# Kernel tuning notes

Hardware: AMD Instinct MI355X
Metric: run time of the kernel (lower is better)

## Reference

```python
import jax, jax.numpy as jnp
import numpy as np

ALPHA = 8.3  # depth similarity sharpness, F_D = exp(-alpha*|D(p0)-D(pn)|) (depth-aware CNN)
PAD, STRIDE, DIL, KH, KW = 1, 1, 1, 3, 3


def setup_inputs() -> dict:
    key = jax.random.key(0)
    k1, k2, k3, k4 = jax.random.split(key, 4)
    B, C_in, C_out, H, W = 2, 32, 32, 512, 512
    x = jax.random.normal(k1, (B, C_in, H, W), dtype=jnp.float32)
    depth = jax.random.uniform(k2, (B, 1, H, W), dtype=jnp.float32)
    weight = jax.random.normal(k3, (C_out, C_in, KH, KW), dtype=jnp.float32) * 0.05
    bias = jax.random.normal(k4, (C_out,), dtype=jnp.float32) * 0.05
    return {"x": x, "depth": depth, "weight": weight, "bias": bias}


def _depthconv(x, depth, weight, bias):
    B, C, H, W = x.shape
    C_out = weight.shape[0]
    H_out = (H + 2 * PAD - DIL * (KH - 1) - 1) // STRIDE + 1
    W_out = (W + 2 * PAD - DIL * (KW - 1) - 1) // STRIDE + 1
    x_p = jnp.pad(x, ((0, 0), (0, 0), (PAD, PAD), (PAD, PAD)))
    d_p = jnp.pad(depth, ((0, 0), (0, 0), (PAD, PAD), (PAD, PAD)))
    # depth at the receptive-field center of each output pixel, [B,1,H_out,W_out]
    ci, cj = (KH // 2) * DIL, (KW // 2) * DIL
    d_c = d_p[:, :, ci:ci + H_out * STRIDE:STRIDE, cj:cj + W_out * STRIDE:STRIDE]
    out = jnp.broadcast_to(bias[None, :, None, None], (B, C_out, H_out, W_out)).astype(x.dtype)
    for ki in range(KH):
        for kj in range(KW):
            hs, ws = ki * DIL, kj * DIL
            xs = x_p[:, :, hs:hs + H_out * STRIDE:STRIDE, ws:ws + W_out * STRIDE:STRIDE]
            ds = d_p[:, :, hs:hs + H_out * STRIDE:STRIDE, ws:ws + W_out * STRIDE:STRIDE]
            sim = jnp.exp(-ALPHA * jnp.abs(d_c - ds))  # [B,1,H_out,W_out]
            out = out + jnp.einsum('oc,bchw->bohw', weight[:, :, ki, kj], xs * sim)
    return out


def reference(x, depth, weight, bias):
    return _depthconv(x, depth, weight, bias)
```

## Files before the change

kernel.cpp:

```cpp
#include <hip/hip_runtime.h>

typedef _Float16 half8 __attribute__((ext_vector_type(8)));
typedef float floatx16 __attribute__((ext_vector_type(16)));

constexpr int C = 32, H = 512, W = 512, HW = H * W;
constexpr int TBW = 32;
constexpr int TBH = 4;
constexpr int RR  = TBH + 2;
constexpr int PX  = TBW + 8;
constexpr int PXW = 20;
constexpr int ROWW = PX * PXW + 4;

__device__ __forceinline__ unsigned pack2h(float lo, float hi) {
    unsigned a = (unsigned)__builtin_bit_cast(unsigned short, (_Float16)lo);
    unsigned b = (unsigned)__builtin_bit_cast(unsigned short, (_Float16)hi);
    return a | (b << 16);
}

__global__ __launch_bounds__(256) void pack_w(const float* __restrict__ weight,
                                              uint4* __restrict__ wp) {
    int j = blockIdx.x * 256 + threadIdx.x;
    if (j >= 1152) return;
    int lane = j & 63, kh = (j >> 6) & 1, tap = j >> 7;
    int m = lane & 31, hh = lane >> 5;
    const float* wb = weight + (size_t)(m * 32 + kh * 16 + hh * 8) * 9 + tap;
    uint4 v;
    v.x = pack2h(wb[0 * 9], wb[1 * 9]);
    v.y = pack2h(wb[2 * 9], wb[3 * 9]);
    v.z = pack2h(wb[4 * 9], wb[5 * 9]);
    v.w = pack2h(wb[6 * 9], wb[7 * 9]);
    wp[j] = v;
}

__global__ __launch_bounds__(256, 4) void depthconv_fused(
    const float* __restrict__ x, const float* __restrict__ depth,
    const uint4* __restrict__ wp, const float* __restrict__ bias,
    float* __restrict__ out)
{
    __shared__ __attribute__((aligned(16))) unsigned xsl[RR * ROWW];

    const int bid  = blockIdx.x;
    const int xcd  = bid & 7, sub = (bid >> 3) & 1;
    const int hseg = (bid >> 4) & 127, b = bid >> 11;
    const int w0 = (xcd * 2 + sub) * TBW, h0 = hseg * TBH;
    const int tid = threadIdx.x;
    const int lane = tid & 63, wid = tid >> 6;
    const int pcl = lane & 31, hh = lane >> 5;

    #pragma unroll
    for (int k = 0; k < 4; ++k) {
        int u = tid + k * 256;
        if (u < 960) {
            int f4 = u % 10, t = u / 10, cp = t & 15, r = t >> 4;
            int h = h0 - 1 + r, wst = w0 - 4 + 4 * f4;
            bool valid = ((unsigned)h < (unsigned)H) && ((unsigned)wst < (unsigned)W);
            float4 va = {0.f, 0.f, 0.f, 0.f}, vb = {0.f, 0.f, 0.f, 0.f};
            if (valid) {
                const float* xb = x + ((size_t)(b * C + 2 * cp)) * HW + (size_t)h * W + wst;
                va = *(const float4*)xb;
                vb = *(const float4*)(xb + HW);
            }
            int word = 4 * ((cp >> 2) ^ ((f4 >> 1) & 3)) + (cp & 3);
            unsigned* dst = &xsl[r * ROWW + (4 * f4) * PXW + word];
            dst[0 * PXW] = pack2h(va.x, vb.x);
            dst[1 * PXW] = pack2h(va.y, vb.y);
            dst[2 * PXW] = pack2h(va.z, vb.z);
            dst[3 * PXW] = pack2h(va.w, vb.w);
        }
    }

    if (tid < RR * PX) {
        int px = tid % PX, r = tid / PX;
        int h = h0 - 1 + r, ww = w0 - 4 + px;
        bool valid = ((unsigned)h < (unsigned)H) && ((unsigned)ww < (unsigned)W);
        float d = valid ? depth[(size_t)b * HW + (size_t)h * W + ww] : 0.f;
        float2 e = valid ? make_float2(__expf(-8.3f * d), __expf(8.3f * d))
                         : make_float2(0.f, 0.f);
        *(float2*)&xsl[r * ROWW + px * PXW + 16] = e;
    }

    floatx16 accA, accB;
    #pragma unroll
    for (int g = 0; g < 4; ++g) {
        float4 bv = *(const float4*)(bias + g * 8 + 4 * hh);
        accA[4 * g + 0] = bv.x; accA[4 * g + 1] = bv.y;
        accA[4 * g + 2] = bv.z; accA[4 * g + 3] = bv.w;
        accB[4 * g + 0] = 0.f;  accB[4 * g + 1] = 0.f;
        accB[4 * g + 2] = 0.f;  accB[4 * g + 3] = 0.f;
    }

    __syncthreads();

    const float2 dc = *(const float2*)&xsl[(wid + 1) * ROWW + (pcl + 4) * PXW + 16];

    #pragma unroll
    for (int ki = 0; ki < 3; ++ki) {
        const unsigned* srow = &xsl[(wid + ki) * ROWW];
        const uint4* wpt = wp + (size_t)(ki * 3) * 128;
        #pragma clang loop unroll(disable)
        for (int kj = 0; kj < 3; ++kj) {
            int p = pcl + 3 + kj;
            int key = (p >> 3) & 3;
            const unsigned* rec = srow + p * PXW;
            uint4 x0 = *(const uint4*)(rec + 4 * (hh ^ key));
            uint4 x1 = *(const uint4*)(rec + 4 * ((2 + hh) ^ key));
            float2 dn = *(const float2*)(rec + 16);
            float s = fminf(dn.y * dc.x, dn.x * dc.y);
            _Float16 hs = (_Float16)s;
            half8 sv = { hs, hs, hs, hs, hs, hs, hs, hs };
            half8 a0 = __builtin_bit_cast(half8, wpt[kj * 128 + lane]);
            half8 a1 = __builtin_bit_cast(half8, wpt[kj * 128 + 64 + lane]);
            accA = __builtin_amdgcn_mfma_f32_32x32x16_f16(
                       a0, __builtin_bit_cast(half8, x0) * sv, accA, 0, 0, 0);
            accB = __builtin_amdgcn_mfma_f32_32x32x16_f16(
                       a1, __builtin_bit_cast(half8, x1) * sv, accB, 0, 0, 0);
        }
    }

    float* op = out + (size_t)b * C * HW + (size_t)(h0 + wid) * W + w0 + pcl;
    #pragma unroll
    for (int i = 0; i < 16; ++i) {
        int ch = (i & 3) + 8 * (i >> 2) + 4 * hh;
        op[(size_t)ch * HW] = accA[i] + accB[i];
    }
}

extern "C" void kernel_launch(void* const* d_in, const int* in_sizes, int n_in,
                              void* d_out, int out_size, void* d_ws, size_t ws_size,
                              hipStream_t stream) {
    const float* x      = (const float*)d_in[0];
    const float* depth  = (const float*)d_in[1];
    const float* weight = (const float*)d_in[2];
    const float* bias   = (const float*)d_in[3];
    float* out          = (float*)d_out;

    uint4* wpk = (uint4*)d_ws;

    hipLaunchKernelGGL(pack_w, dim3(5), dim3(256), 0, stream, weight, wpk);
    hipLaunchKernelGGL(depthconv_fused, dim3(4096), dim3(256), 0, stream,
                       x, depth, wpk, bias, out);
}
```

Measured before the change: 144.9 us.

## Prefetch weights and tile loads into registers, software-pipeline LDS reads in MFMA loop

All 18 weight fragments are loaded into registers up front instead of inside the tap loop. The global x and depth loads are issued first as clamped, unconditional loads, and the fp16 packing and LDS stores happen afterwards, so the memory loads can overlap. The tap loop is fully unrolled, precomputes the nine depth similarity scalars, and double-buffers the LDS reads of x so the next tap's data is fetched during the current MFMAs. Register pressure rises sharply, so the occupancy hint is lowered from 4 to 3 blocks per CU.

```diff
diff --git a/kernel.cpp b/kernel.cpp
--- a/kernel.cpp
+++ b/kernel.cpp
@@ -32,7 +32,7 @@
     wp[j] = v;
 }
 
-__global__ __launch_bounds__(256, 4) void depthconv_fused(
+__global__ __launch_bounds__(256, 3) void depthconv_fused(
     const float* __restrict__ x, const float* __restrict__ depth,
     const uint4* __restrict__ wp, const float* __restrict__ bias,
     float* __restrict__ out)
@@ -47,36 +47,59 @@
     const int lane = tid & 63, wid = tid >> 6;
     const int pcl = lane & 31, hh = lane >> 5;
 
+    half8 afA[9], afB[9];
+    #pragma unroll
+    for (int t = 0; t < 9; ++t) {
+        afA[t] = __builtin_bit_cast(half8, wp[t * 128 + lane]);
+        afB[t] = __builtin_bit_cast(half8, wp[t * 128 + 64 + lane]);
+    }
+
+    float4 va[4], vb[4];
+    bool okk[4], hask[4];
+    int f4k[4], cpk[4], rk[4];
     #pragma unroll
     for (int k = 0; k < 4; ++k) {
         int u = tid + k * 256;
-        if (u < 960) {
-            int f4 = u % 10, t = u / 10, cp = t & 15, r = t >> 4;
-            int h = h0 - 1 + r, wst = w0 - 4 + 4 * f4;
-            bool valid = ((unsigned)h < (unsigned)H) && ((unsigned)wst < (unsigned)W);
-            float4 va = {0.f, 0.f, 0.f, 0.f}, vb = {0.f, 0.f, 0.f, 0.f};
-            if (valid) {
-                const float* xb = x + ((size_t)(b * C + 2 * cp)) * HW + (size_t)h * W + wst;
-                va = *(const float4*)xb;
-                vb = *(const float4*)(xb + HW);
-            }
-            int word = 4 * ((cp >> 2) ^ ((f4 >> 1) & 3)) + (cp & 3);
-            unsigned* dst = &xsl[r * ROWW + (4 * f4) * PXW + word];
-            dst[0 * PXW] = pack2h(va.x, vb.x);
-            dst[1 * PXW] = pack2h(va.y, vb.y);
-            dst[2 * PXW] = pack2h(va.z, vb.z);
-            dst[3 * PXW] = pack2h(va.w, vb.w);
-        }
+        bool has = (k < 3) || (tid < 192);
+        int f4 = u % 10, t = u / 10, cp = t & 15, r = t >> 4;
+        f4k[k] = f4; cpk[k] = cp; rk[k] = r; hask[k] = has;
+        int h = h0 - 1 + r, wst = w0 - 4 + 4 * f4;
+        okk[k] = ((unsigned)h < (unsigned)H) && ((unsigned)wst < (unsigned)W);
+        int hc = h < 0 ? 0 : (h > H - 1 ? H - 1 : h);
+        int wc = wst < 0 ? 0 : (wst > W - 4 ? W - 4 : wst);
+        const float* xb = x + ((size_t)(b * C + 2 * cp)) * HW + (size_t)hc * W + wc;
+        va[k] = *(const float4*)xb;
+        vb[k] = *(const float4*)(xb + HW);
     }
 
+    float dval = 0.f; bool dok = false; int dpx = 0, dr = 0;
+    {
+        int u = tid;
+        int px = u % PX, r = u / PX;
+        dpx = px; dr = r;
+        int h = h0 - 1 + r, ww = w0 - 4 + px;
+        dok = (u < RR * PX) && ((unsigned)h < (unsigned)H) && ((unsigned)ww < (unsigned)W);
+        int hc = h < 0 ? 0 : (h > H - 1 ? H - 1 : h);
+        int wc = ww < 0 ? 0 : (ww > W - 1 ? W - 1 : ww);
+        dval = depth[(size_t)b * HW + (size_t)hc * W + wc];
+    }
+
+    #pragma unroll
+    for (int k = 0; k < 4; ++k) {
+        if (k == 3 && tid >= 192) continue;
+        float4 A = va[k], B = vb[k];
+        if (!okk[k]) { A = make_float4(0,0,0,0); B = make_float4(0,0,0,0); }
+        int word = 4 * ((cpk[k] >> 2) ^ ((f4k[k] >> 1) & 3)) + (cpk[k] & 3);
+        unsigned* dst = &xsl[rk[k] * ROWW + (4 * f4k[k]) * PXW + word];
+        dst[0 * PXW] = pack2h(A.x, B.x);
+        dst[1 * PXW] = pack2h(A.y, B.y);
+        dst[2 * PXW] = pack2h(A.z, B.z);
+        dst[3 * PXW] = pack2h(A.w, B.w);
+    }
     if (tid < RR * PX) {
-        int px = tid % PX, r = tid / PX;
-        int h = h0 - 1 + r, ww = w0 - 4 + px;
-        bool valid = ((unsigned)h < (unsigned)H) && ((unsigned)ww < (unsigned)W);
-        float d = valid ? depth[(size_t)b * HW + (size_t)h * W + ww] : 0.f;
-        float2 e = valid ? make_float2(__expf(-8.3f * d), __expf(8.3f * d))
-                         : make_float2(0.f, 0.f);
-        *(float2*)&xsl[r * ROWW + px * PXW + 16] = e;
+        float2 e = dok ? make_float2(__expf(-8.3f * dval), __expf(8.3f * dval))
+                       : make_float2(0.f, 0.f);
+        *(float2*)&xsl[dr * ROWW + dpx * PXW + 16] = e;
     }
 
     floatx16 accA, accB;
@@ -92,29 +115,34 @@
     __syncthreads();
 
     const float2 dc = *(const float2*)&xsl[(wid + 1) * ROWW + (pcl + 4) * PXW + 16];
+    float2 dnv[9];
+    #pragma unroll
+    for (int t = 0; t < 9; ++t) {
+        int ki = t / 3, kj = t % 3, p = pcl + 3 + kj;
+        dnv[t] = *(const float2*)&xsl[(wid + ki) * ROWW + p * PXW + 16];
+    }
+    _Float16 sh[9];
+    #pragma unroll
+    for (int t = 0; t < 9; ++t)
+        sh[t] = (_Float16)fminf(dnv[t].y * dc.x, dnv[t].x * dc.y);
 
+    auto rdx = [&](int t, int g) -> uint4 {
+        int ki = t / 3, kj = t % 3, p = pcl + 3 + kj, key = (p >> 3) & 3;
+        const unsigned* rec = &xsl[(wid + ki) * ROWW + p * PXW];
+        return *(const uint4*)(rec + 4 * (g ^ key));
+    };
+    uint4 c0 = rdx(0, hh), c1 = rdx(0, 2 + hh);
     #pragma unroll
-    for (int ki = 0; ki < 3; ++ki) {
-        const unsigned* srow = &xsl[(wid + ki) * ROWW];
-        const uint4* wpt = wp + (size_t)(ki * 3) * 128;
-        #pragma clang loop unroll(disable)
-        for (int kj = 0; kj < 3; ++kj) {
-            int p = pcl + 3 + kj;
-            int key = (p >> 3) & 3;
-            const unsigned* rec = srow + p * PXW;
-            uint4 x0 = *(const uint4*)(rec + 4 * (hh ^ key));
-            uint4 x1 = *(const uint4*)(rec + 4 * ((2 + hh) ^ key));
-            float2 dn = *(const float2*)(rec + 16);
-            float s = fminf(dn.y * dc.x, dn.x * dc.y);
-            _Float16 hs = (_Float16)s;
-            half8 sv = { hs, hs, hs, hs, hs, hs, hs, hs };
-            half8 a0 = __builtin_bit_cast(half8, wpt[kj * 128 + lane]);
-            half8 a1 = __builtin_bit_cast(half8, wpt[kj * 128 + 64 + lane]);
-            accA = __builtin_amdgcn_mfma_f32_32x32x16_f16(
-                       a0, __builtin_bit_cast(half8, x0) * sv, accA, 0, 0, 0);
-            accB = __builtin_amdgcn_mfma_f32_32x32x16_f16(
-                       a1, __builtin_bit_cast(half8, x1) * sv, accB, 0, 0, 0);
-        }
+    for (int t = 0; t < 9; ++t) {
+        uint4 n0, n1;
+        if (t < 8) { n0 = rdx(t + 1, hh); n1 = rdx(t + 1, 2 + hh); }
+        _Float16 hs = sh[t];
+        half8 sv = { hs, hs, hs, hs, hs, hs, hs, hs };
+        accA = __builtin_amdgcn_mfma_f32_32x32x16_f16(
+                   afA[t], __builtin_bit_cast(half8, c0) * sv, accA, 0, 0, 0);
+        accB = __builtin_amdgcn_mfma_f32_32x32x16_f16(
+                   afB[t], __builtin_bit_cast(half8, c1) * sv, accB, 0, 0, 0);
+        c0 = n0; c1 = n1;
     }
 
     float* op = out + (size_t)b * C * HW + (size_t)(h0 + wid) * W + w0 + pcl;
```

New measurement: 148.8 us. 2.6% more time.
